# Kernel optimization log

Hardware: AMD Instinct MI355X
Metric: run time of the kernel (lower is better)

The kernel has to match this reference:

```python
import jax, jax.numpy as jnp
import numpy as np

B, S, D = 8, 1024, 256
H = 8            # num_heads
HD = D // H      # head_dim
FF = 1024        # expert hidden_dim
E = 8            # num_experts
K = 2            # top-k
L = 2            # num_layers
OUT = 1000       # output_dim
EPS = 1e-5


def setup_inputs() -> dict:
    key = jax.random.key(0)
    ks = jax.random.split(key, 20)
    std = 0.02
    inp = {
        "x": jax.random.normal(ks[0], (B, S, D), jnp.float32),
        "qkv_w": jax.random.normal(ks[1], (L, D, 3 * D), jnp.float32) * std,
        "qkv_b": jnp.zeros((L, 3 * D), jnp.float32),
        "attn_w": jax.random.normal(ks[2], (L, D, D), jnp.float32) * std,
        "attn_b": jnp.zeros((L, D), jnp.float32),
        "gate_w": jax.random.normal(ks[3], (L, D, E), jnp.float32) * std,
        "gate_b": jnp.zeros((L, E), jnp.float32),
        "e_w1": jax.random.normal(ks[4], (L, E, D, FF), jnp.float32) * std,
        "e_b1": jnp.zeros((L, E, FF), jnp.float32),
        "e_w2": jax.random.normal(ks[5], (L, E, FF, D), jnp.float32) * std,
        "e_b2": jnp.zeros((L, E, D), jnp.float32),
        "ln1_g": jnp.ones((D,), jnp.float32),
        "ln1_b": jnp.zeros((D,), jnp.float32),
        "ln2_g": jnp.ones((D,), jnp.float32),
        "ln2_b": jnp.zeros((D,), jnp.float32),
        "head_w": jax.random.normal(ks[6], (D, OUT), jnp.float32) * std,
        "head_b": jnp.zeros((OUT,), jnp.float32),
    }
    return inp


def _layer_norm(x, g, b):
    m = jnp.mean(x, -1, keepdims=True)
    v = jnp.mean((x - m) ** 2, -1, keepdims=True)
    return (x - m) / jnp.sqrt(v + EPS) * g + b


def _attention(x, w_qkv, b_qkv, w_o, b_o):
    # x: [B,S,D]
    qkv = (x @ w_qkv + b_qkv).reshape(B, S, 3, H, HD)
    q, k, v = jnp.moveaxis(qkv, 2, 0)            # each [B,S,H,HD]
    q = q.transpose(0, 2, 1, 3)                   # [B,H,S,HD]
    k = k.transpose(0, 2, 1, 3)
    v = v.transpose(0, 2, 1, 3)
    attn = jax.nn.softmax(jnp.einsum('bhqd,bhkd->bhqk', q, k) * (HD ** -0.5), axis=-1)
    o = jnp.einsum('bhqk,bhkd->bhqd', attn, v).transpose(0, 2, 1, 3).reshape(B, S, D)
    return o @ w_o + b_o


def _moe(x, gw, gb, w1, b1, w2, b2):
    # x: [B,S,D] -> tokens [T,D]
    xf = x.reshape(-1, D)
    gates = xf @ gw + gb                           # [T,E]
    scores, idx = jax.lax.top_k(gates, K)          # [T,K]
    gate_w = jax.nn.softmax(scores, axis=-1)       # [T,K]
    # dense all-expert compute, then gather selected experts per token
    h = jax.nn.gelu(jnp.einsum('td,edh->teh', xf, w1) + b1, approximate=False)
    eo = jnp.einsum('teh,ehd->ted', h, w2) + b2    # [T,E,D]
    sel = jnp.take_along_axis(eo, idx[:, :, None], axis=1)  # [T,K,D]
    out = jnp.sum(gate_w[:, :, None] * sel, axis=1)
    return out.reshape(B, S, D)


def reference(x, qkv_w, qkv_b, attn_w, attn_b, gate_w, gate_b,
              e_w1, e_b1, e_w2, e_b2, ln1_g, ln1_b, ln2_g, ln2_b,
              head_w, head_b):
    for l in range(L):
        x = x + _attention(_layer_norm(x, ln1_g, ln1_b),
                           qkv_w[l], qkv_b[l], attn_w[l], attn_b[l])
        x = x + _moe(_layer_norm(x, ln2_g, ln2_b),
                     gate_w[l], gate_b[l], e_w1[l], e_b1[l], e_w2[l], e_b2[l])
    pooled = jnp.mean(x, axis=1)                   # [B,D]
    return pooled @ head_w + head_b                # [B,OUT]
```

## Files before the change

### kernel.cpp

```cpp
#include <hip/hip_runtime.h>
#include <math.h>

#define TOK   8192
#define DIM   256
#define NH    8
#define HDIM  32
#define FFD   1024
#define NE    8
#define NL    2
#define NOUT  1000
#define NSLOT 16384

typedef unsigned int uint;
typedef unsigned short ushort;
typedef __attribute__((ext_vector_type(8))) short short8;
typedef __attribute__((ext_vector_type(4))) float f32x4;

#define WS_X     ((size_t)0)
#define WS_LN    (WS_X    + (size_t)TOK*DIM)
#define WS_QKV   (WS_LN   + (size_t)TOK*DIM)
#define WS_H     (WS_QKV  + (size_t)TOK*3*DIM)
#define WS_SOUT  (WS_H    + (size_t)NSLOT*256)
#define WS_GV    (WS_SOUT + (size_t)NSLOT*256)
#define WS_PP    (WS_GV   + (size_t)TOK*2)
#define WS_POOL  (WS_PP   + (size_t)8*32*256)
#define WS_INT   (WS_POOL + (size_t)8*256)
#define WS_U16   (WS_INT  + (size_t)54144)
#define WS_BIG   (WS_U16  + (size_t)2359296)

#define IB_COUNTS   0
#define IB_NTILES   8
#define IB_OFFS     16
#define IB_CURS     24
#define IB_TILE_E   32
#define IB_TILE_R0  320
#define IB_TILE_RE  608
#define IB_GIDX     896
#define IB_SPOS     17280
#define IB_STOK     33664
#define IB_BLKC     50048
#define IB_BLKB     52096

__device__ __forceinline__ float gelu_exact(float v) {
    float z = v * 0.70710678118654752f;
    float s = fabsf(z);
    float t = __builtin_amdgcn_rcpf(1.0f + 0.3275911f * s);
    float p = ((((1.061405429f * t - 1.453152027f) * t + 1.421413741f) * t
                - 0.284496736f) * t + 0.254829592f) * t;
    float r = 1.0f - p * __expf(-s * s);
    float er = (z < 0.0f) ? -r : r;
    return 0.5f * v * (1.0f + er);
}

__device__ __forceinline__ ushort rnd_bf16(float x) {
    uint u = __float_as_uint(x);
    return (ushort)((u + 0x7FFFu + ((u >> 16) & 1u)) >> 16);
}

__device__ __forceinline__ void split2(float x, ushort& h, ushort& lo) {
    uint u = __float_as_uint(x);
    uint hh = (u + 0x7FFFu + ((u >> 16) & 1u)) >> 16;
    h = (ushort)hh;
    float hf = __uint_as_float(hh << 16);
    float l = x - hf;
    uint ul = __float_as_uint(l);
    lo = (ushort)((ul + 0x7FFFu + ((ul >> 16) & 1u)) >> 16);
}

__device__ __forceinline__ void gld16(const ushort* g, ushort* l) {
    __builtin_amdgcn_global_load_lds(
        (const __attribute__((address_space(1))) uint*)g,
        (__attribute__((address_space(3))) uint*)l, 16, 0, 0);
}

__device__ __forceinline__ void xcd_map(int bid, int NC, int& t, int& j) {
    int g = bid >> 3;
    t = (bid & 7) + 8 * (g / NC);
    j = g % NC;
}

template<bool WF32>
__global__ __launch_bounds__(256) void ln_split(const float* __restrict__ x,
                                                float* __restrict__ out,
                                                ushort* __restrict__ ohi,
                                                const float* __restrict__ g,
                                                const float* __restrict__ b) {
    int wave = threadIdx.x >> 6;
    int lane = threadIdx.x & 63;
    int t = blockIdx.x * 4 + wave;
    const float* xp = x + (size_t)t * DIM;
    float4 v = *(const float4*)&xp[lane * 4];
    float s = v.x + v.y + v.z + v.w;
    #pragma unroll
    for (int off = 32; off; off >>= 1) s += __shfl_xor(s, off);
    float mean = s * (1.0f / 256.0f);
    float dx = v.x - mean, dy = v.y - mean, dz = v.z - mean, dw = v.w - mean;
    float vs = dx * dx + dy * dy + dz * dz + dw * dw;
    #pragma unroll
    for (int off = 32; off; off >>= 1) vs += __shfl_xor(vs, off);
    float inv = rsqrtf(vs * (1.0f / 256.0f) + 1e-5f);
    float4 gg = *(const float4*)&g[lane * 4];
    float4 bb = *(const float4*)&b[lane * 4];
    float o0 = dx * inv * gg.x + bb.x;
    float o1 = dy * inv * gg.y + bb.y;
    float o2 = dz * inv * gg.z + bb.z;
    float o3 = dw * inv * gg.w + bb.w;
    size_t idx = (size_t)t * DIM + lane * 4;
    if (WF32) {
        float4 o; o.x = o0; o.y = o1; o.z = o2; o.w = o3;
        *(float4*)&out[idx] = o;
    }
    uint2 ph;
    ph.x = (uint)rnd_bf16(o0) | ((uint)rnd_bf16(o1) << 16);
    ph.y = (uint)rnd_bf16(o2) | ((uint)rnd_bf16(o3) << 16);
    *(uint2*)&ohi[idx] = ph;
}

template<bool WLO>
__global__ __launch_bounds__(256) void split_transpose(const float* __restrict__ src,
                                                       ushort* __restrict__ dhi,
                                                       ushort* __restrict__ dlo,
                                                       int K, int N) {
    int z = blockIdx.z;
    const float* s = src + (size_t)z * K * N;
    ushort* th = dhi + (size_t)z * K * N;
    ushort* tl = dlo + (size_t)z * K * N;
    __shared__ float tile[32][33];
    int k0 = blockIdx.x * 32, n0 = blockIdx.y * 32;
    int tx = threadIdx.x & 31, ty = threadIdx.x >> 5;
    #pragma unroll
    for (int i = 0; i < 4; ++i) {
        int k = k0 + ty + i * 8;
        tile[ty + i * 8][tx] = s[(size_t)k * N + n0 + tx];
    }
    __syncthreads();
    #pragma unroll
    for (int i = 0; i < 4; ++i) {
        int n = n0 + ty + i * 8;
        float v = tile[tx][ty + i * 8];
        ushort h, lo;
        split2(v, h, lo);
        th[(size_t)n * K + k0 + tx] = h;
        if (WLO) tl[(size_t)n * K + k0 + tx] = lo;
    }
}


template<int MODE>
__global__ __launch_bounds__(256) void mfma_dense128x64(const ushort* __restrict__ Ah,
                                                        const ushort* __restrict__ Bh,
                                                        const float* __restrict__ bias,
                                                        float* __restrict__ C,
                                                        ushort* __restrict__ Chi, int N, int NC) {
    __shared__ ushort LAh[128][64], LBh[64][64];
    int tT, tJ;
    xcd_map(blockIdx.x, NC, tT, tJ);
    int tid = threadIdx.x;
    int w = tid >> 6, l = tid & 63, c = l & 15, G = l >> 4;
    int row0 = tT * 128, col0 = tJ * 64;
    int lr = l >> 3, sd = l & 7;
    size_t gaA[4]; ushort* dA[4];
    size_t gbB[2]; ushort* dB[2];
    #pragma unroll
    for (int i = 0; i < 4; ++i) {
        int r = i * 32 + w * 8 + lr;
        gaA[i] = (size_t)(row0 + r) * 256 + ((sd ^ (r & 7)) << 3);
        dA[i] = &LAh[i * 32 + w * 8][0];
    }
    #pragma unroll
    for (int i = 0; i < 2; ++i) {
        int r = i * 32 + w * 8 + lr;
        gbB[i] = (size_t)(col0 + r) * 256 + ((sd ^ (r & 7)) << 3);
        dB[i] = &LBh[i * 32 + w * 8][0];
    }
    f32x4 acc[2][4] = {};
    for (int k0 = 0; k0 < 256; k0 += 64) {
        #pragma unroll
        for (int i = 0; i < 4; ++i) gld16(&Ah[gaA[i] + k0], dA[i]);
        #pragma unroll
        for (int i = 0; i < 2; ++i) gld16(&Bh[gbB[i] + k0], dB[i]);
        __syncthreads();
        #pragma unroll
        for (int s = 0; s < 2; ++s) {
            int ar = w * 32 + c;
            short8 a_h[2];
            #pragma unroll
            for (int i = 0; i < 2; ++i) {
                int r = ar + i * 16;
                int sg = (((s << 2) | G) ^ (r & 7)) << 3;
                a_h[i] = *(const short8*)&LAh[r][sg];
            }
            #pragma unroll
            for (int j = 0; j < 4; ++j) {
                int r = j * 16 + c;
                int sg = (((s << 2) | G) ^ (r & 7)) << 3;
                short8 b_h = *(const short8*)&LBh[r][sg];
                #pragma unroll
                for (int i = 0; i < 2; ++i) {
                    acc[i][j] = __builtin_amdgcn_mfma_f32_16x16x32_bf16(a_h[i], b_h, acc[i][j], 0, 0, 0);
                }
            }
        }
        __syncthreads();
    }
    int rbase = row0 + w * 32 + G * 4;
    #pragma unroll
    for (int i = 0; i < 2; ++i) {
        #pragma unroll
        for (int j = 0; j < 4; ++j) {
            int gc = col0 + j * 16 + c;
            float bv = bias[gc];
            #pragma unroll
            for (int rr = 0; rr < 4; ++rr) {
                int grow = rbase + i * 16 + rr;
                size_t idx = (size_t)grow * N + gc;
                float v = acc[i][j][rr] + bv;
                if (MODE == 1) v += C[idx];
                if (MODE == 3) {
                    Chi[idx] = rnd_bf16(v);
                } else {
                    C[idx] = v;
                }
            }
        }
    }
}

__global__ __launch_bounds__(256) void vt_kernel(const ushort* __restrict__ qkvh,
                                                 ushort* __restrict__ vth) {
    int bh = blockIdx.y;
    int b = bh >> 3, h = bh & 7;
    int kv0 = blockIdx.x * 32;
    __shared__ ushort smh[32][33];
    int tid = threadIdx.x;
    #pragma unroll
    for (int p = 0; p < 4; ++p) {
        int kv = p * 8 + (tid >> 5);
        int d = tid & 31;
        size_t src = ((size_t)(b * 1024 + kv0 + kv)) * 768 + 512 + h * 32 + d;
        smh[kv][d] = qkvh[src];
    }
    __syncthreads();
    #pragma unroll
    for (int p = 0; p < 4; ++p) {
        int d = p * 8 + (tid >> 5);
        int kv = tid & 31;
        size_t dst = ((size_t)(bh * 32 + d)) * 1024 + kv0 + kv;
        vth[dst] = smh[kv][d];
    }
}

__global__ __launch_bounds__(256, 4) void attention_mfma(const ushort* __restrict__ qkvh,
                                                         const ushort* __restrict__ vth,
                                                         ushort* __restrict__ ohi) {
    int b = blockIdx.z, h = blockIdx.y;
    int q0 = blockIdx.x * 64;
    int tid = threadIdx.x;
    int w = tid >> 6, l = tid & 63;
    int c = l & 15, g = l >> 4;
    __shared__ ushort Kh[128][40];
    __shared__ ushort VTh[32][136];
    __shared__ ushort Ph[4][16][140];

    size_t qbase = ((size_t)(b * 1024 + q0 + w * 16 + c)) * 768 + h * 32 + g * 8;
    short8 qa_h = *(const short8*)&qkvh[qbase];

    f32x4 acc_o[2] = {};
    float lpart[4] = {0.f, 0.f, 0.f, 0.f};
    const float scale = 0.17677669529663687f;

    int sr = tid >> 2, sc8 = (tid & 3) * 8;
    size_t kgbase = ((size_t)(b * 1024 + sr)) * 768 + 256 + h * 32 + sc8;
    int vd = tid >> 4, vk8 = (tid & 15) * 8;
    size_t vtbase = ((size_t)((b * 8 + h) * 32 + vd)) * 1024 + vk8;

    uint4 k0r = *(const uint4*)&qkvh[kgbase];
    uint4 k1r = *(const uint4*)&qkvh[kgbase + (size_t)64 * 768];
    uint4 v0r = *(const uint4*)&vth[vtbase];
    uint4 v1r = *(const uint4*)&vth[vtbase + 16 * 1024];

    for (int kv0 = 0; kv0 < 1024; kv0 += 128) {
        __syncthreads();
        *(uint4*)&Kh[sr][sc8]       = k0r;
        *(uint4*)&Kh[sr + 64][sc8]  = k1r;
        *(uint4*)&VTh[vd][vk8]      = v0r;
        *(uint4*)&VTh[vd + 16][vk8] = v1r;
        __syncthreads();

        if (kv0 + 128 < 1024) {
            k0r = *(const uint4*)&qkvh[kgbase + (size_t)(kv0 + 128) * 768];
            k1r = *(const uint4*)&qkvh[kgbase + (size_t)(kv0 + 192) * 768];
            v0r = *(const uint4*)&vth[vtbase + kv0 + 128];
            v1r = *(const uint4*)&vth[vtbase + 16 * 1024 + kv0 + 128];
        }

        f32x4 s4[8];
        #pragma unroll
        for (int t = 0; t < 8; ++t) {
            short8 kh = *(const short8*)&Kh[t * 16 + c][g * 8];
            f32x4 a = {};
            a = __builtin_amdgcn_mfma_f32_16x16x32_bf16(qa_h, kh, a, 0, 0, 0);
            s4[t] = a;
        }

        #pragma unroll
        for (int rr = 0; rr < 4; ++rr) {
            float sum = 0.f;
            #pragma unroll
            for (int t = 0; t < 8; ++t) {
                float p = __expf(s4[t][rr] * scale);
                uint u = __float_as_uint(p);
                uint r = (u + 0x7FFFu + ((u >> 16) & 1u)) >> 16;
                Ph[w][g * 4 + rr][t * 16 + c] = (ushort)r;
                sum += __uint_as_float(r << 16);
            }
            lpart[rr] += sum;
        }
        asm volatile("s_waitcnt lgkmcnt(0)" ::: "memory");

        #pragma unroll
        for (int kt = 0; kt < 4; ++kt) {
            short8 pah = *(const short8*)&Ph[w][c][kt * 32 + g * 8];
            #pragma unroll
            for (int T = 0; T < 2; ++T) {
                short8 vh = *(const short8*)&VTh[T * 16 + c][kt * 32 + g * 8];
                acc_o[T] = __builtin_amdgcn_mfma_f32_16x16x32_bf16(pah, vh, acc_o[T], 0, 0, 0);
            }
        }
    }

    #pragma unroll
    for (int rr = 0; rr < 4; ++rr) {
        float s = lpart[rr];
        s += __shfl_xor(s, 1);
        s += __shfl_xor(s, 2);
        s += __shfl_xor(s, 4);
        s += __shfl_xor(s, 8);
        lpart[rr] = s;
    }

    #pragma unroll
    for (int rr = 0; rr < 4; ++rr) {
        float inv = 1.0f / lpart[rr];
        int q = q0 + w * 16 + g * 4 + rr;
        #pragma unroll
        for (int T = 0; T < 2; ++T) {
            float v = acc_o[T][rr] * inv;
            size_t idx = (size_t)(b * 1024 + q) * 256 + h * 32 + T * 16 + c;
            ohi[idx] = rnd_bf16(v);
        }
    }
}

__global__ __launch_bounds__(256) void mfma_ffn1_12864(const ushort* __restrict__ Ah,
                                                       const ushort* __restrict__ W1h,
                                                       const float* __restrict__ b1l,
                                                       ushort* __restrict__ hh,
                                                       const int* __restrict__ ib,
                                                       int c0, int hFF, int NC) {
    int tileIdx, cj;
    xcd_map(blockIdx.x, NC, tileIdx, cj);
    if (tileIdx >= ib[IB_NTILES]) return;
    int e = ib[IB_TILE_E + tileIdx];
    int row0 = ib[IB_TILE_R0 + tileIdx];
    int rowend = ib[IB_TILE_RE + tileIdx];
    __shared__ ushort LAh[128][64], LBh[64][64];
    __shared__ int tok[128];
    int tid = threadIdx.x;
    if (tid < 128) {
        int sr = row0 + tid;
        tok[tid] = ib[IB_STOK + (sr < rowend ? sr : row0)];
    }
    __syncthreads();
    int w = tid >> 6, l = tid & 63, c = l & 15, G = l >> 4;
    int lr = l >> 3, sd = l & 7;
    int colbase = cj * 64;
    const ushort* Bh = W1h + (size_t)e * 262144 + (size_t)(c0 + colbase) * 256;
    size_t gaA[4]; ushort* dA[4];
    size_t gbB[2]; ushort* dB[2];
    #pragma unroll
    for (int i = 0; i < 4; ++i) {
        int r = i * 32 + w * 8 + lr;
        gaA[i] = (size_t)tok[r] * 256 + ((sd ^ (r & 7)) << 3);
        dA[i] = &LAh[i * 32 + w * 8][0];
    }
    #pragma unroll
    for (int i = 0; i < 2; ++i) {
        int r = i * 32 + w * 8 + lr;
        gbB[i] = (size_t)r * 256 + ((sd ^ (r & 7)) << 3);
        dB[i] = &LBh[i * 32 + w * 8][0];
    }
    f32x4 acc[2][4] = {};
    for (int k0 = 0; k0 < 256; k0 += 64) {
        #pragma unroll
        for (int i = 0; i < 4; ++i) gld16(&Ah[gaA[i] + k0], dA[i]);
        #pragma unroll
        for (int i = 0; i < 2; ++i) gld16(&Bh[gbB[i] + k0], dB[i]);
        __syncthreads();
        #pragma unroll
        for (int s = 0; s < 2; ++s) {
            int ar = w * 32 + c;
            short8 a_h[2];
            #pragma unroll
            for (int i = 0; i < 2; ++i) {
                int r = ar + i * 16;
                int sg = (((s << 2) | G) ^ (r & 7)) << 3;
                a_h[i] = *(const short8*)&LAh[r][sg];
            }
            #pragma unroll
            for (int j = 0; j < 4; ++j) {
                int r = j * 16 + c;
                int sg = (((s << 2) | G) ^ (r & 7)) << 3;
                short8 b_h = *(const short8*)&LBh[r][sg];
                #pragma unroll
                for (int i = 0; i < 2; ++i) {
                    acc[i][j] = __builtin_amdgcn_mfma_f32_16x16x32_bf16(a_h[i], b_h, acc[i][j], 0, 0, 0);
                }
            }
        }
        __syncthreads();
    }
    int rbase = row0 + w * 32 + G * 4;
    #pragma unroll
    for (int i = 0; i < 2; ++i) {
        #pragma unroll
        for (int j = 0; j < 4; ++j) {
            int cl = colbase + j * 16 + c;
            float bv = b1l[(size_t)e * FFD + c0 + cl];
            #pragma unroll
            for (int rr = 0; rr < 4; ++rr) {
                int sr = rbase + i * 16 + rr;
                if (sr < rowend) {
                    float v = gelu_exact(acc[i][j][rr] + bv);
                    hh[(size_t)sr * hFF + cl] = rnd_bf16(v);
                }
            }
        }
    }
}

__global__ __launch_bounds__(256) void mfma_ffn2_12864(const ushort* __restrict__ Ah,
                                                       const ushort* __restrict__ W2h,
                                                       const float* __restrict__ b2l,
                                                       float* __restrict__ sout,
                                                       const int* __restrict__ ib,
                                                       int c0, int hFF, int NC) {
    int tileIdx, cj;
    xcd_map(blockIdx.x, NC, tileIdx, cj);
    if (tileIdx >= ib[IB_NTILES]) return;
    int e = ib[IB_TILE_E + tileIdx];
    int row0 = ib[IB_TILE_R0 + tileIdx];
    int rowend = ib[IB_TILE_RE + tileIdx];
    __shared__ ushort LAh[128][64], LBh[64][64];
    int tid = threadIdx.x;
    int w = tid >> 6, l = tid & 63, c = l & 15, G = l >> 4;
    int lr = l >> 3, sd = l & 7;
    int colbase = cj * 64;
    const ushort* Bh = W2h + (size_t)e * 262144;
    size_t gaA[4]; ushort* dA[4];
    size_t gbB[2]; ushort* dB[2];
    #pragma unroll
    for (int i = 0; i < 4; ++i) {
        int r = i * 32 + w * 8 + lr;
        gaA[i] = (size_t)(row0 + r) * hFF + ((sd ^ (r & 7)) << 3);
        dA[i] = &LAh[i * 32 + w * 8][0];
    }
    #pragma unroll
    for (int i = 0; i < 2; ++i) {
        int r = i * 32 + w * 8 + lr;
        gbB[i] = (size_t)(colbase + r) * 1024 + c0 + ((sd ^ (r & 7)) << 3);
        dB[i] = &LBh[i * 32 + w * 8][0];
    }
    f32x4 acc[2][4] = {};
    for (int k0 = 0; k0 < hFF; k0 += 64) {
        #pragma unroll
        for (int i = 0; i < 4; ++i) gld16(&Ah[gaA[i] + k0], dA[i]);
        #pragma unroll
        for (int i = 0; i < 2; ++i) gld16(&Bh[gbB[i] + k0], dB[i]);
        __syncthreads();
        #pragma unroll
        for (int s = 0; s < 2; ++s) {
            int ar = w * 32 + c;
            short8 a_h[2];
            #pragma unroll
            for (int i = 0; i < 2; ++i) {
                int r = ar + i * 16;
                int sg = (((s << 2) | G) ^ (r & 7)) << 3;
                a_h[i] = *(const short8*)&LAh[r][sg];
            }
            #pragma unroll
            for (int j = 0; j < 4; ++j) {
                int r = j * 16 + c;
                int sg = (((s << 2) | G) ^ (r & 7)) << 3;
                short8 b_h = *(const short8*)&LBh[r][sg];
                #pragma unroll
                for (int i = 0; i < 2; ++i) {
                    acc[i][j] = __builtin_amdgcn_mfma_f32_16x16x32_bf16(a_h[i], b_h, acc[i][j], 0, 0, 0);
                }
            }
        }
        __syncthreads();
    }
    int rbase = row0 + w * 32 + G * 4;
    #pragma unroll
    for (int i = 0; i < 2; ++i) {
        #pragma unroll
        for (int j = 0; j < 4; ++j) {
            int n = colbase + j * 16 + c;
            float bv = b2l[(size_t)e * DIM + n];
            #pragma unroll
            for (int rr = 0; rr < 4; ++rr) {
                int sr = rbase + i * 16 + rr;
                if (sr < rowend) {
                    size_t idx = (size_t)sr * 256 + n;
                    if (c0 == 0) sout[idx] = acc[i][j][rr] + bv;
                    else         sout[idx] += acc[i][j][rr];
                }
            }
        }
    }
}

__global__ __launch_bounds__(256) void gate_topk(const float* __restrict__ lnb,
                                                 const float* __restrict__ gw,
                                                 const float* __restrict__ gb,
                                                 float* __restrict__ gv, int* __restrict__ ib) {
    __shared__ int hist[8];
    int tid = threadIdx.x;
    if (tid < 8) hist[tid] = 0;
    __syncthreads();
    int grp = tid >> 3, ln8 = tid & 7;
    int t = blockIdx.x * 32 + grp;
    const float* x = lnb + (size_t)t * DIM + ln8 * 32;
    const float* wb = gw + (size_t)ln8 * 32 * 8;
    float g[8] = {};
    #pragma unroll
    for (int d4 = 0; d4 < 8; ++d4) {
        float4 xv = *(const float4*)&x[d4 * 4];
        const float* wr = wb + d4 * 32;
        float4 wa0 = *(const float4*)&wr[0],  wb0 = *(const float4*)&wr[4];
        float4 wa1 = *(const float4*)&wr[8],  wb1 = *(const float4*)&wr[12];
        float4 wa2 = *(const float4*)&wr[16], wb2 = *(const float4*)&wr[20];
        float4 wa3 = *(const float4*)&wr[24], wb3 = *(const float4*)&wr[28];
        g[0] += xv.x * wa0.x + xv.y * wa1.x + xv.z * wa2.x + xv.w * wa3.x;
        g[1] += xv.x * wa0.y + xv.y * wa1.y + xv.z * wa2.y + xv.w * wa3.y;
        g[2] += xv.x * wa0.z + xv.y * wa1.z + xv.z * wa2.z + xv.w * wa3.z;
        g[3] += xv.x * wa0.w + xv.y * wa1.w + xv.z * wa2.w + xv.w * wa3.w;
        g[4] += xv.x * wb0.x + xv.y * wb1.x + xv.z * wb2.x + xv.w * wb3.x;
        g[5] += xv.x * wb0.y + xv.y * wb1.y + xv.z * wb2.y + xv.w * wb3.y;
        g[6] += xv.x * wb0.z + xv.y * wb1.z + xv.z * wb2.z + xv.w * wb3.z;
        g[7] += xv.x * wb0.w + xv.y * wb1.w + xv.z * wb2.w + xv.w * wb3.w;
    }
    #pragma unroll
    for (int e = 0; e < 8; ++e) {
        g[e] += __shfl_xor(g[e], 1);
        g[e] += __shfl_xor(g[e], 2);
        g[e] += __shfl_xor(g[e], 4);
    }
    if (ln8 == 0) {
        #pragma unroll
        for (int e = 0; e < 8; ++e) g[e] += gb[e];
        int i0 = 0; float s0 = g[0];
        #pragma unroll
        for (int e = 1; e < 8; ++e) if (g[e] > s0) { s0 = g[e]; i0 = e; }
        int i1 = -1; float s1 = -1e30f;
        #pragma unroll
        for (int e = 0; e < 8; ++e) if (e != i0 && g[e] > s1) { s1 = g[e]; i1 = e; }
        float e1 = __expf(s1 - s0);
        float w0v = 1.0f / (1.0f + e1);
        float w1v = e1 / (1.0f + e1);
        gv[2 * t] = w0v; gv[2 * t + 1] = w1v;
        ib[IB_GIDX + 2 * t] = i0; ib[IB_GIDX + 2 * t + 1] = i1;
        atomicAdd(&hist[i0], 1);
        atomicAdd(&hist[i1], 1);
    }
    __syncthreads();
    if (tid < 8) ib[IB_BLKC + blockIdx.x * 8 + tid] = hist[tid];
}

__global__ __launch_bounds__(256) void scan_tiles(int* ib) {
    __shared__ int bc[2048], bb[2048];
    __shared__ int counts[8], offs[8], tstart[9];
    int tid = threadIdx.x;
    for (int i = tid; i < 2048; i += 256) bc[i] = ib[IB_BLKC + i];
    __syncthreads();
    if (tid < 8) {
        int run = 0;
        for (int b = 0; b < 256; ++b) {
            bb[b * 8 + tid] = run;
            run += bc[b * 8 + tid];
        }
        counts[tid] = run;
    }
    __syncthreads();
    if (tid == 0) {
        int off = 0, ts = 0;
        for (int e = 0; e < 8; ++e) {
            offs[e] = off;
            ib[IB_OFFS + e] = off;
            tstart[e] = ts;
            ib[IB_COUNTS + e] = counts[e];
            ts += (counts[e] + 127) >> 7;
            off += counts[e];
        }
        tstart[8] = ts;
        ib[IB_NTILES] = ts;
    }
    __syncthreads();
    for (int i = tid; i < 2048; i += 256)
        ib[IB_BLKB + i] = offs[i & 7] + bb[i];
    int total = tstart[8];
    for (int idx = tid; idx < total; idx += 256) {
        int e = 0;
        while (idx >= tstart[e + 1]) ++e;
        int i = idx - tstart[e];
        ib[IB_TILE_E + idx] = e;
        ib[IB_TILE_R0 + idx] = offs[e] + i * 128;
        int rem = counts[e] - i * 128;
        ib[IB_TILE_RE + idx] = offs[e] + i * 128 + (rem < 128 ? rem : 128);
    }
}

__global__ __launch_bounds__(64) void scatter_slots(int* ib) {
    __shared__ int cnt8[8];
    int tid = threadIdx.x;
    if (tid < 8) cnt8[tid] = ib[IB_BLKB + blockIdx.x * 8 + tid];
    __syncthreads();
    int t = blockIdx.x * 32 + (tid >> 1);
    int k = tid & 1;
    int e = ib[IB_GIDX + 2 * t + k];
    int pos = atomicAdd(&cnt8[e], 1);
    ib[IB_STOK + pos] = t;
    ib[IB_SPOS + 2 * t + k] = pos;
}

__global__ __launch_bounds__(64) void moe_gather(float* __restrict__ xb,
                                                 const float* __restrict__ sout,
                                                 const float* __restrict__ gv,
                                                 const int* __restrict__ ib) {
    int t = blockIdx.x;
    int d = threadIdx.x * 4;
    int p0 = ib[IB_SPOS + 2 * t], p1 = ib[IB_SPOS + 2 * t + 1];
    float g0 = gv[2 * t], g1 = gv[2 * t + 1];
    float4 xv = *(float4*)&xb[(size_t)t * 256 + d];
    float4 s0 = *(const float4*)&sout[(size_t)p0 * 256 + d];
    float4 s1 = *(const float4*)&sout[(size_t)p1 * 256 + d];
    xv.x += g0 * s0.x + g1 * s1.x;
    xv.y += g0 * s0.y + g1 * s1.y;
    xv.z += g0 * s0.z + g1 * s1.z;
    xv.w += g0 * s0.w + g1 * s1.w;
    *(float4*)&xb[(size_t)t * 256 + d] = xv;
}

__global__ __launch_bounds__(256) void pool1(const float* __restrict__ xb, float* __restrict__ pp) {
    int b = blockIdx.x, ch = blockIdx.y, d = threadIdx.x;
    float s = 0.0f;
    for (int i = 0; i < 32; ++i) s += xb[((size_t)b * 1024 + ch * 32 + i) * 256 + d];
    pp[(size_t)(b * 32 + ch) * 256 + d] = s;
}
__global__ __launch_bounds__(256) void pool2(const float* __restrict__ pp, float* __restrict__ pool) {
    int b = blockIdx.x, d = threadIdx.x;
    float s = 0.0f;
    for (int c = 0; c < 32; ++c) s += pp[(size_t)(b * 32 + c) * 256 + d];
    pool[(size_t)b * 256 + d] = s * (1.0f / 1024.0f);
}

__global__ __launch_bounds__(256) void head_kernel(const float* __restrict__ pool,
                                                   const float* __restrict__ hw,
                                                   const float* __restrict__ hb,
                                                   float* __restrict__ out) {
    __shared__ float P[2048];
    int tid = threadIdx.x;
    for (int i = tid; i < 2048; i += 256) P[i] = pool[i];
    __syncthreads();
    int j = blockIdx.x * 256 + tid;
    if (j >= NOUT) return;
    float acc[8] = {};
    for (int d = 0; d < 256; ++d) {
        float w = hw[(size_t)d * NOUT + j];
        #pragma unroll
        for (int b = 0; b < 8; ++b) acc[b] += P[b * 256 + d] * w;
    }
    #pragma unroll
    for (int b = 0; b < 8; ++b) out[(size_t)b * NOUT + j] = acc[b] + hb[j];
}

extern "C" void kernel_launch(void* const* d_in, const int* in_sizes, int n_in,
                              void* d_out, int out_size, void* d_ws, size_t ws_size,
                              hipStream_t stream) {
    const float* x      = (const float*)d_in[0];
    const float* qkv_w  = (const float*)d_in[1];
    const float* qkv_b  = (const float*)d_in[2];
    const float* attn_w = (const float*)d_in[3];
    const float* attn_b = (const float*)d_in[4];
    const float* gate_w = (const float*)d_in[5];
    const float* gate_b = (const float*)d_in[6];
    const float* e_w1   = (const float*)d_in[7];
    const float* e_b1   = (const float*)d_in[8];
    const float* e_w2   = (const float*)d_in[9];
    const float* e_b2   = (const float*)d_in[10];
    const float* ln1_g  = (const float*)d_in[11];
    const float* ln1_b  = (const float*)d_in[12];
    const float* ln2_g  = (const float*)d_in[13];
    const float* ln2_b  = (const float*)d_in[14];
    const float* head_w = (const float*)d_in[15];
    const float* head_b = (const float*)d_in[16];
    float* out = (float*)d_out;
    float* wsf = (float*)d_ws;

    float* xb   = wsf + WS_X;
    float* lnb  = wsf + WS_LN;
    float* sob  = wsf + WS_SOUT;
    float* gv   = wsf + WS_GV;
    float* pp   = wsf + WS_PP;
    float* pool = wsf + WS_POOL;
    int*   ib   = (int*)(wsf + WS_INT);

    ushort* qkvsh = (ushort*)(wsf + WS_QKV);
    ushort* wT    = (ushort*)(wsf + WS_QKV);
    ushort* w1th  = wT;
    ushort* w2th  = wT + 4194304;
    ushort* wTdummy = wT + 6291456;

    ushort* vth = (ushort*)(wsf + WS_H);

    ushort* u16  = (ushort*)(wsf + WS_U16);
    ushort* lnh  = u16;
    ushort* qwh  = u16 + 4194304;
    ushort* awh  = u16 + 4587520;

    size_t base_bytes = (size_t)WS_BIG * 4;
    int hFF = 256;
    if (ws_size >= base_bytes + (size_t)NSLOT * 1024 * 2)      hFF = 1024;
    else if (ws_size >= base_bytes + (size_t)NSLOT * 512 * 2)  hFF = 512;
    ushort* hh = (hFF == 256) ? (ushort*)(wsf + WS_H) : (ushort*)(wsf + WS_BIG);
    int NCC = 1024 / hFF;

    hipMemcpyAsync(xb, x, (size_t)TOK * DIM * sizeof(float), hipMemcpyDeviceToDevice, stream);

    for (int l = 0; l < NL; ++l) {
        ln_split<false><<<TOK / 4, 256, 0, stream>>>(xb, nullptr, lnh, ln1_g, ln1_b);
        split_transpose<false><<<dim3(8, 24, 1), 256, 0, stream>>>(
            qkv_w + (size_t)l * DIM * 3 * DIM, qwh, wTdummy, 256, 768);
        mfma_dense128x64<3><<<64 * 12, 256, 0, stream>>>(
            lnh, qwh, qkv_b + (size_t)l * 3 * DIM, nullptr, qkvsh, 768, 12);
        vt_kernel<<<dim3(32, 64), 256, 0, stream>>>(qkvsh, vth);
        attention_mfma<<<dim3(16, NH, 8), 256, 0, stream>>>(qkvsh, vth, lnh);
        split_transpose<false><<<dim3(8, 8, 1), 256, 0, stream>>>(
            attn_w + (size_t)l * DIM * DIM, awh, wTdummy, 256, 256);
        mfma_dense128x64<1><<<64 * 4, 256, 0, stream>>>(
            lnh, awh, attn_b + (size_t)l * DIM, xb, nullptr, 256, 4);

        ln_split<true><<<TOK / 4, 256, 0, stream>>>(xb, lnb, lnh, ln2_g, ln2_b);
        split_transpose<false><<<dim3(8, 32, 8), 256, 0, stream>>>(
            e_w1 + (size_t)l * NE * DIM * FFD, w1th, wTdummy, 256, 1024);
        split_transpose<false><<<dim3(32, 8, 8), 256, 0, stream>>>(
            e_w2 + (size_t)l * NE * FFD * DIM, w2th, wTdummy, 1024, 256);
        gate_topk<<<TOK / 32, 256, 0, stream>>>(
            lnb, gate_w + (size_t)l * DIM * NE, gate_b + (size_t)l * NE, gv, ib);
        scan_tiles<<<1, 256, 0, stream>>>(ib);
        scatter_slots<<<TOK / 32, 64, 0, stream>>>(ib);
        for (int c = 0; c < NCC; ++c) {
            mfma_ffn1_12864<<<136 * (hFF / 64), 256, 0, stream>>>(
                lnh, w1th, e_b1 + (size_t)l * NE * FFD, hh, ib, c * hFF, hFF, hFF / 64);
            mfma_ffn2_12864<<<136 * 4, 256, 0, stream>>>(
                hh, w2th, e_b2 + (size_t)l * NE * DIM, sob, ib, c * hFF, hFF, 4);
        }
        moe_gather<<<TOK, 64, 0, stream>>>(xb, sob, gv, ib);
    }

    pool1<<<dim3(8, 32), 256, 0, stream>>>(xb, pp);
    pool2<<<8, 256, 0, stream>>>(pp, pool);
    head_kernel<<<4, 256, 0, stream>>>(pool, head_w, head_b, out);
}
```

Before: 332.5 us.

## Fuse weight transposes and fold next-layer LayerNorm into MoE gather

Merges the QKV and output-projection weight split-transposes into one launch, and the two expert-weight transposes into another. It drops the unused low-part computation from the transpose kernels. The next layer's LN1 is computed inside moe_gather for every layer except the last, which removes one ln_split launch and one reread of x. Together these cut the kernel launch count and some memory traffic. The cost is slightly more work inside the gather kernel.

```diff
diff --git a/kernel.cpp b/kernel.cpp
--- a/kernel.cpp
+++ b/kernel.cpp
@@ -57,16 +57,6 @@
     return (ushort)((u + 0x7FFFu + ((u >> 16) & 1u)) >> 16);
 }
 
-__device__ __forceinline__ void split2(float x, ushort& h, ushort& lo) {
-    uint u = __float_as_uint(x);
-    uint hh = (u + 0x7FFFu + ((u >> 16) & 1u)) >> 16;
-    h = (ushort)hh;
-    float hf = __uint_as_float(hh << 16);
-    float l = x - hf;
-    uint ul = __float_as_uint(l);
-    lo = (ushort)((ul + 0x7FFFu + ((ul >> 16) & 1u)) >> 16);
-}
-
 __device__ __forceinline__ void gld16(const ushort* g, ushort* l) {
     __builtin_amdgcn_global_load_lds(
         (const __attribute__((address_space(1))) uint*)g,
@@ -116,17 +106,16 @@
     *(uint2*)&ohi[idx] = ph;
 }
 
-template<bool WLO>
-__global__ __launch_bounds__(256) void split_transpose(const float* __restrict__ src,
-                                                       ushort* __restrict__ dhi,
-                                                       ushort* __restrict__ dlo,
-                                                       int K, int N) {
-    int z = blockIdx.z;
-    const float* s = src + (size_t)z * K * N;
-    ushort* th = dhi + (size_t)z * K * N;
-    ushort* tl = dlo + (size_t)z * K * N;
+__global__ __launch_bounds__(256) void st_attn_weights(const float* __restrict__ qkvw,
+                                                       const float* __restrict__ attnw,
+                                                       ushort* __restrict__ qwh,
+                                                       ushort* __restrict__ awh) {
     __shared__ float tile[32][33];
-    int k0 = blockIdx.x * 32, n0 = blockIdx.y * 32;
+    int y = blockIdx.y;
+    const float* s; ushort* th; int N, n0;
+    int K = 256, k0 = blockIdx.x * 32;
+    if (y < 24) { s = qkvw;  th = qwh; N = 768; n0 = y * 32; }
+    else        { s = attnw; th = awh; N = 256; n0 = (y - 24) * 32; }
     int tx = threadIdx.x & 31, ty = threadIdx.x >> 5;
     #pragma unroll
     for (int i = 0; i < 4; ++i) {
@@ -137,11 +126,37 @@
     #pragma unroll
     for (int i = 0; i < 4; ++i) {
         int n = n0 + ty + i * 8;
-        float v = tile[tx][ty + i * 8];
-        ushort h, lo;
-        split2(v, h, lo);
-        th[(size_t)n * K + k0 + tx] = h;
-        if (WLO) tl[(size_t)n * K + k0 + tx] = lo;
+        th[(size_t)n * K + k0 + tx] = rnd_bf16(tile[tx][ty + i * 8]);
+    }
+}
+
+__global__ __launch_bounds__(256) void st_expert_weights(const float* __restrict__ w1,
+                                                         const float* __restrict__ w2,
+                                                         ushort* __restrict__ w1th,
+                                                         ushort* __restrict__ w2th) {
+    __shared__ float tile[32][33];
+    int z = blockIdx.y;
+    int idx = blockIdx.x;
+    const float* s; ushort* th; int K, N, k0, n0;
+    if (idx < 256) {
+        s = w1 + (size_t)z * 262144; th = w1th + (size_t)z * 262144;
+        K = 256; N = 1024; k0 = (idx & 7) * 32; n0 = (idx >> 3) * 32;
+    } else {
+        idx -= 256;
+        s = w2 + (size_t)z * 262144; th = w2th + (size_t)z * 262144;
+        K = 1024; N = 256; k0 = (idx & 31) * 32; n0 = (idx >> 5) * 32;
+    }
+    int tx = threadIdx.x & 31, ty = threadIdx.x >> 5;
+    #pragma unroll
+    for (int i = 0; i < 4; ++i) {
+        int k = k0 + ty + i * 8;
+        tile[ty + i * 8][tx] = s[(size_t)k * N + n0 + tx];
+    }
+    __syncthreads();
+    #pragma unroll
+    for (int i = 0; i < 4; ++i) {
+        int n = n0 + ty + i * 8;
+        th[(size_t)n * K + k0 + tx] = rnd_bf16(tile[tx][ty + i * 8]);
     }
 }
 
@@ -634,10 +649,14 @@
     ib[IB_SPOS + 2 * t + k] = pos;
 }
 
+template<bool WLN>
 __global__ __launch_bounds__(64) void moe_gather(float* __restrict__ xb,
                                                  const float* __restrict__ sout,
                                                  const float* __restrict__ gv,
-                                                 const int* __restrict__ ib) {
+                                                 const int* __restrict__ ib,
+                                                 ushort* __restrict__ ohi,
+                                                 const float* __restrict__ g,
+                                                 const float* __restrict__ b) {
     int t = blockIdx.x;
     int d = threadIdx.x * 4;
     int p0 = ib[IB_SPOS + 2 * t], p1 = ib[IB_SPOS + 2 * t + 1];
@@ -650,6 +669,27 @@
     xv.z += g0 * s0.z + g1 * s1.z;
     xv.w += g0 * s0.w + g1 * s1.w;
     *(float4*)&xb[(size_t)t * 256 + d] = xv;
+    if (WLN) {
+        float s = xv.x + xv.y + xv.z + xv.w;
+        #pragma unroll
+        for (int off = 32; off; off >>= 1) s += __shfl_xor(s, off);
+        float mean = s * (1.0f / 256.0f);
+        float dx = xv.x - mean, dy = xv.y - mean, dz = xv.z - mean, dw = xv.w - mean;
+        float vs = dx * dx + dy * dy + dz * dz + dw * dw;
+        #pragma unroll
+        for (int off = 32; off; off >>= 1) vs += __shfl_xor(vs, off);
+        float inv = rsqrtf(vs * (1.0f / 256.0f) + 1e-5f);
+        float4 gg = *(const float4*)&g[d];
+        float4 bb = *(const float4*)&b[d];
+        float o0 = dx * inv * gg.x + bb.x;
+        float o1 = dy * inv * gg.y + bb.y;
+        float o2 = dz * inv * gg.z + bb.z;
+        float o3 = dw * inv * gg.w + bb.w;
+        uint2 ph;
+        ph.x = (uint)rnd_bf16(o0) | ((uint)rnd_bf16(o1) << 16);
+        ph.y = (uint)rnd_bf16(o2) | ((uint)rnd_bf16(o3) << 16);
+        *(uint2*)&ohi[(size_t)t * 256 + d] = ph;
+    }
 }
 
 __global__ __launch_bounds__(256) void pool1(const float* __restrict__ xb, float* __restrict__ pp) {
@@ -720,7 +760,6 @@
     ushort* wT    = (ushort*)(wsf + WS_QKV);
     ushort* w1th  = wT;
     ushort* w2th  = wT + 4194304;
-    ushort* wTdummy = wT + 6291456;
 
     ushort* vth = (ushort*)(wsf + WS_H);
 
@@ -739,23 +778,20 @@
     hipMemcpyAsync(xb, x, (size_t)TOK * DIM * sizeof(float), hipMemcpyDeviceToDevice, stream);
 
     for (int l = 0; l < NL; ++l) {
-        ln_split<false><<<TOK / 4, 256, 0, stream>>>(xb, nullptr, lnh, ln1_g, ln1_b);
-        split_transpose<false><<<dim3(8, 24, 1), 256, 0, stream>>>(
-            qkv_w + (size_t)l * DIM * 3 * DIM, qwh, wTdummy, 256, 768);
+        if (l == 0)
+            ln_split<false><<<TOK / 4, 256, 0, stream>>>(xb, nullptr, lnh, ln1_g, ln1_b);
+        st_attn_weights<<<dim3(8, 32), 256, 0, stream>>>(
+            qkv_w + (size_t)l * DIM * 3 * DIM, attn_w + (size_t)l * DIM * DIM, qwh, awh);
         mfma_dense128x64<3><<<64 * 12, 256, 0, stream>>>(
             lnh, qwh, qkv_b + (size_t)l * 3 * DIM, nullptr, qkvsh, 768, 12);
         vt_kernel<<<dim3(32, 64), 256, 0, stream>>>(qkvsh, vth);
         attention_mfma<<<dim3(16, NH, 8), 256, 0, stream>>>(qkvsh, vth, lnh);
-        split_transpose<false><<<dim3(8, 8, 1), 256, 0, stream>>>(
-            attn_w + (size_t)l * DIM * DIM, awh, wTdummy, 256, 256);
         mfma_dense128x64<1><<<64 * 4, 256, 0, stream>>>(
             lnh, awh, attn_b + (size_t)l * DIM, xb, nullptr, 256, 4);
 
         ln_split<true><<<TOK / 4, 256, 0, stream>>>(xb, lnb, lnh, ln2_g, ln2_b);
-        split_transpose<false><<<dim3(8, 32, 8), 256, 0, stream>>>(
-            e_w1 + (size_t)l * NE * DIM * FFD, w1th, wTdummy, 256, 1024);
-        split_transpose<false><<<dim3(32, 8, 8), 256, 0, stream>>>(
-            e_w2 + (size_t)l * NE * FFD * DIM, w2th, wTdummy, 1024, 256);
+        st_expert_weights<<<dim3(512, 8), 256, 0, stream>>>(
+            e_w1 + (size_t)l * NE * DIM * FFD, e_w2 + (size_t)l * NE * FFD * DIM, w1th, w2th);
         gate_topk<<<TOK / 32, 256, 0, stream>>>(
             lnb, gate_w + (size_t)l * DIM * NE, gate_b + (size_t)l * NE, gv, ib);
         scan_tiles<<<1, 256, 0, stream>>>(ib);
@@ -766,7 +802,10 @@
             mfma_ffn2_12864<<<136 * 4, 256, 0, stream>>>(
                 hh, w2th, e_b2 + (size_t)l * NE * DIM, sob, ib, c * hFF, hFF, 4);
         }
-        moe_gather<<<TOK, 64, 0, stream>>>(xb, sob, gv, ib);
+        if (l + 1 < NL)
+            moe_gather<true><<<TOK, 64, 0, stream>>>(xb, sob, gv, ib, lnh, ln1_g, ln1_b);
+        else
+            moe_gather<false><<<TOK, 64, 0, stream>>>(xb, sob, gv, ib, nullptr, nullptr, nullptr);
     }
 
     pool1<<<dim3(8, 32), 256, 0, stream>>>(xb, pp);
```

Measured after the change: 322.1 us. 1.03x faster.
